# Kernel tuning notes

Measured on AMD Instinct MI355X. Metric: run time of the kernel, lower is better.

## Reference

```python
import jax, jax.numpy as jnp
import numpy as np

B, L, E = 4, 1024, 1024
H, TOPK = 16, 32
DH = E // H


def setup_inputs() -> dict:
    key = jax.random.key(0)
    ks = jax.random.split(key, 11)
    s = 1.0 / np.sqrt(E)
    return {
        "Q": jax.random.normal(ks[0], (B, L, E), jnp.float32),
        "K": jax.random.normal(ks[1], (B, L, E), jnp.float32),
        "V": jax.random.normal(ks[2], (B, L, E), jnp.float32),
        "Wq": jax.random.normal(ks[3], (E, E), jnp.float32) * s,
        "bq": jnp.zeros((E,), jnp.float32),
        "Wk": jax.random.normal(ks[4], (E, E), jnp.float32) * s,
        "bk": jnp.zeros((E,), jnp.float32),
        "Wv": jax.random.normal(ks[5], (E, E), jnp.float32) * s,
        "bv": jnp.zeros((E,), jnp.float32),
        "Wo": jax.random.normal(ks[6], (E, E), jnp.float32) * s,
        "bo": jnp.zeros((E,), jnp.float32),
    }


def reference(Q, K, V, Wq, bq, Wk, bk, Wv, bv, Wo, bo):
    # Linear projections (torch Linear: x @ W.T + b), split heads -> [B,H,L,Dh]
    q = (Q @ Wq.T + bq).reshape(B, L, H, DH).transpose(0, 2, 1, 3)
    k = (K @ Wk.T + bk).reshape(B, L, H, DH).transpose(0, 2, 1, 3)
    v = (V @ Wv.T + bv).reshape(B, L, H, DH).transpose(0, 2, 1, 3)

    # Full attention logits [B,H,L,L]
    logits = jnp.einsum("bhld,bhmd->bhlm", q, k) / np.sqrt(DH)

    # Keep only top-k per query row; rest -> -inf (as in torch scatter_)
    top_vals, top_idx = jax.lax.top_k(logits, TOPK)  # [B,H,L,TOPK]
    bi = jnp.arange(B)[:, None, None, None]
    hi = jnp.arange(H)[None, :, None, None]
    li = jnp.arange(L)[None, None, :, None]
    masked = jnp.full_like(logits, -jnp.inf).at[bi, hi, li, top_idx].set(top_vals)

    attn = jax.nn.softmax(masked, axis=-1)
    out = jnp.einsum("bhlm,bhmd->bhld", attn, v)
    out = out.transpose(0, 2, 1, 3).reshape(B, L, E)
    return out @ Wo.T + bo
```

## Files before the change

kernel.cpp:

```cpp
#include <hip/hip_runtime.h>


typedef short v8s __attribute__((ext_vector_type(8)));
typedef _Float16 v8h __attribute__((ext_vector_type(8)));
typedef float v4f __attribute__((ext_vector_type(4)));

#define B_ 4
#define L_ 1024
#define E_ 1024
#define H_ 16
#define DH_ 64
#define M_ 4096

__device__ __forceinline__ unsigned short f2bf_u(float f) {
    unsigned u = __float_as_uint(f);
    unsigned r = u + 0x7FFFu + ((u >> 16) & 1u);
    return (unsigned short)(r >> 16);
}
__device__ __forceinline__ unsigned short f2h_u(float f) {
    _Float16 h = (_Float16)f;
    union { _Float16 h; unsigned short u; } c; c.h = h; return c.u;
}
__device__ __forceinline__ float h2f_u(unsigned short u) {
    union { _Float16 h; unsigned short u; } c; c.u = u; return (float)c.h;
}
__device__ __forceinline__ unsigned f2key(float f) {
    unsigned u = __float_as_uint(f);
    u = ((int)u < 0) ? ~u : (u | 0x80000000u);
    return u & 0xFFFFFFF0u;
}
__device__ __forceinline__ unsigned f2keyfull(float f) {
    unsigned u = __float_as_uint(f);
    return ((int)u < 0) ? ~u : (u | 0x80000000u);
}
__device__ __forceinline__ float key2f(unsigned k) {
    unsigned u = (k & 0x80000000u) ? (k & 0x7FFFFFFFu) : ~k;
    return __uint_as_float(u);
}
__device__ __forceinline__ float rl_f(float v, int l) {
    return __uint_as_float((unsigned)__builtin_amdgcn_readlane(__float_as_int(v), l));
}
__device__ __forceinline__ int rl_i(int v, int l) {
    return __builtin_amdgcn_readlane(v, l);
}
__device__ __forceinline__ void gload_lds16(const unsigned short* g, unsigned short* l) {
    __builtin_amdgcn_global_load_lds(
        (const __attribute__((address_space(1))) void*)g,
        (__attribute__((address_space(3))) void*)l, 16, 0, 0);
}

__global__ __launch_bounds__(256) void splitH_kernel(
    const float* __restrict__ x, unsigned short* __restrict__ y,
    int n8, int isB, float prescale)
{
    int i = blockIdx.x * 256 + threadIdx.x;
    if (i >= n8) return;
    float4 v0 = *(const float4*)(x + 8*(size_t)i);
    float4 v1 = *(const float4*)(x + 8*(size_t)i + 4);
    float f[8] = {v0.x, v0.y, v0.z, v0.w, v1.x, v1.y, v1.z, v1.w};
    unsigned short o[24];
#pragma unroll
    for (int c = 0; c < 8; ++c) {
        float fv = f[c] * prescale;
        unsigned short h = f2h_u(fv);
        float r = fv - h2f_u(h);
        unsigned short l = f2h_u(r);
        int b = 3*c;
        if (!isB) { o[b] = h; o[b+1] = l; o[b+2] = h; }
        else      { o[b] = h; o[b+1] = h; o[b+2] = l; }
    }
    uint4* dst = (uint4*)(y + 24*(size_t)i);
    const unsigned* ou = (const unsigned*)o;
    dst[0] = make_uint4(ou[0], ou[1], ou[2], ou[3]);
    dst[1] = make_uint4(ou[4], ou[5], ou[6], ou[7]);
    dst[2] = make_uint4(ou[8], ou[9], ou[10], ou[11]);
}

#define STAGE_TILE_GEN(Ap_, Bp_, Abuf_, Bbuf_, kt_)                       \
  {                                                                       \
    const int k0_ = (kt_) << 6;                                           \
    _Pragma("unroll")                                                     \
    for (int c_ = 0; c_ < 2; ++c_) {                                      \
      int lin_ = c_*512 + t;                                              \
      int r_ = lin_ >> 3, s_ = lin_ & 7;                                  \
      gload_lds16(Ap_ + (size_t)(m0 + r_)*K2 + k0_ + ((s_ ^ (r_&7))*8),   \
                  &Abuf_[lin_*8]);                                        \
    }                                                                     \
    _Pragma("unroll")                                                     \
    for (int c_ = 0; c_ < 2; ++c_) {                                      \
      int lin_ = c_*512 + t;                                              \
      int r_ = lin_ >> 3, s_ = lin_ & 7;                                  \
      gload_lds16(Bp_ + (size_t)(n0 + r_)*K2 + k0_ + ((s_ ^ (r_&7))*8),   \
                  &Bbuf_[lin_*8]);                                        \
    }                                                                     \
  }

#define GEMM_COMPUTE(Abuf_, Bbuf_)                                        \
  {                                                                       \
    _Pragma("unroll")                                                     \
    for (int ks = 0; ks < 2; ++ks) {                                      \
        v8h af[2], bf[4];                                                 \
        _Pragma("unroll")                                                 \
        for (int mt = 0; mt < 2; ++mt) {                                  \
            int ra = wrow + mt*16 + l16;                                  \
            int sl = (ks*4 + quad) ^ (ra & 7);                            \
            af[mt] = *(const v8h*)&Abuf_[ra*64 + sl*8];                   \
        }                                                                 \
        _Pragma("unroll")                                                 \
        for (int nt = 0; nt < 4; ++nt) {                                  \
            int rb = wcol + nt*16 + l16;                                  \
            int sl = (ks*4 + quad) ^ (rb & 7);                            \
            bf[nt] = *(const v8h*)&Bbuf_[rb*64 + sl*8];                   \
        }                                                                 \
        _Pragma("unroll")                                                 \
        for (int mt = 0; mt < 2; ++mt)                                    \
            _Pragma("unroll")                                             \
            for (int nt = 0; nt < 4; ++nt)                                \
                acc[mt][nt] = __builtin_amdgcn_mfma_f32_16x16x32_f16(     \
                    af[mt], bf[nt], acc[mt][nt], 0, 0, 0);                \
    }                                                                     \
  }

__global__ __launch_bounds__(512) void gemm_f16(
    const unsigned short* __restrict__ A,
    const unsigned short* __restrict__ Bw,
    const float* __restrict__ bias,
    int K2, int mode, float scale,
    float* __restrict__ outF,
    unsigned short* __restrict__ outB)
{
    __shared__ __align__(16) unsigned short As[3][128*64];
    __shared__ __align__(16) unsigned short Bs[3][128*64];
    const int t    = threadIdx.x;
    const int lane = t & 63;
    const int w    = t >> 6;
    const int quad = lane >> 4;
    const int l16  = lane & 15;
    const int bid  = blockIdx.x;
    const int xcd  = bid & 7;
    const int loc  = bid >> 3;
    const int m0   = (xcd * 4 + (loc & 3)) * 128;
    const int n0   = (loc >> 2) * 128;
    const int wrow = (w >> 1) * 32;
    const int wcol = (w & 1) * 64;

    v4f acc[2][4];
#pragma unroll
    for (int i = 0; i < 2; ++i)
#pragma unroll
        for (int j = 0; j < 4; ++j) acc[i][j] = (v4f){0.f,0.f,0.f,0.f};

    STAGE_TILE_GEN(A, Bw, As[0], Bs[0], 0)
    STAGE_TILE_GEN(A, Bw, As[1], Bs[1], 1)

    const int nk = K2 >> 6;
    for (int ki = 0; ki < nk; ++ki) {
        const int cur = ki % 3;
        asm volatile("s_waitcnt lgkmcnt(0)" ::: "memory");
        __builtin_amdgcn_s_barrier();
        if (ki + 2 < nk) {
            const int nb = (ki + 2) % 3;
            STAGE_TILE_GEN(A, Bw, As[nb], Bs[nb], ki + 2)
        }
        if (ki + 2 < nk)       asm volatile("s_waitcnt vmcnt(8)" ::: "memory");
        else if (ki + 1 < nk)  asm volatile("s_waitcnt vmcnt(4)" ::: "memory");
        else                   asm volatile("s_waitcnt vmcnt(0)" ::: "memory");
        __builtin_amdgcn_s_barrier();
        GEMM_COMPUTE(As[cur], Bs[cur])
    }

#pragma unroll
    for (int nt = 0; nt < 4; ++nt) {
        int n = n0 + wcol + nt*16 + l16;
        float bb = bias[n];
#pragma unroll
        for (int mt = 0; mt < 2; ++mt) {
#pragma unroll
            for (int r = 0; r < 4; ++r) {
                int m = m0 + wrow + mt*16 + quad*4 + r;
                float val = (acc[mt][nt][r] * 0.03125f + bb) * scale;
                if (mode == 0) {
                    outF[(size_t)m * 1024 + n] = val;
                } else {
                    int b = m >> 10, l = m & 1023;
                    int h = n >> 6,  d = n & 63;
                    size_t oidx = (((size_t)(b*16 + h)) * 1024 + l) * 64 + d;
                    outF[oidx] = val;
                    if (mode == 2) outB[oidx] = f2bf_u(val);
                }
            }
        }
    }
}

__global__ __launch_bounds__(512, 4) void gemm_f16_qk(
    const unsigned short* __restrict__ A0,
    const unsigned short* __restrict__ A1,
    const unsigned short* __restrict__ B0,
    const unsigned short* __restrict__ B1,
    const float* __restrict__ bias0,
    const float* __restrict__ bias1,
    float scale0, float scale1,
    float* __restrict__ outF0,
    float* __restrict__ outF1,
    unsigned short* __restrict__ outB0,
    unsigned short* __restrict__ outB1)
{
    __shared__ __align__(16) unsigned short As[2][128*64];
    __shared__ __align__(16) unsigned short Bs[2][128*64];
    const int K2   = 3072;
    const int t    = threadIdx.x;
    const int lane = t & 63;
    const int w    = t >> 6;
    const int quad = lane >> 4;
    const int l16  = lane & 15;
    const int z    = blockIdx.y;
    const unsigned short* A  = z ? A1 : A0;
    const unsigned short* Bw = z ? B1 : B0;
    const float* bias        = z ? bias1 : bias0;
    const float scale        = z ? scale1 : scale0;
    float* outF              = z ? outF1 : outF0;
    unsigned short* outB     = z ? outB1 : outB0;

    const int bid  = blockIdx.x;
    const int xcd  = bid & 7;
    const int loc  = bid >> 3;
    const int m0   = (xcd * 4 + (loc & 3)) * 128;
    const int n0   = (loc >> 2) * 128;
    const int wrow = (w >> 1) * 32;
    const int wcol = (w & 1) * 64;

    v4f acc[2][4];
#pragma unroll
    for (int i = 0; i < 2; ++i)
#pragma unroll
        for (int j = 0; j < 4; ++j) acc[i][j] = (v4f){0.f,0.f,0.f,0.f};

    STAGE_TILE_GEN(A, Bw, As[0], Bs[0], 0)

    const int nk = K2 >> 6;
    for (int ki = 0; ki < nk; ++ki) {
        const int cur = ki & 1;
        __syncthreads();
        if (ki + 1 < nk) {
            STAGE_TILE_GEN(A, Bw, As[cur ^ 1], Bs[cur ^ 1], ki + 1)
        }
        GEMM_COMPUTE(As[cur], Bs[cur])
    }

#pragma unroll
    for (int nt = 0; nt < 4; ++nt) {
        int n = n0 + wcol + nt*16 + l16;
        float bb = bias[n];
#pragma unroll
        for (int mt = 0; mt < 2; ++mt) {
#pragma unroll
            for (int r = 0; r < 4; ++r) {
                int m = m0 + wrow + mt*16 + quad*4 + r;
                float val = (acc[mt][nt][r] * 0.03125f + bb) * scale;
                int b = m >> 10, l = m & 1023;
                int h = n >> 6,  d = n & 63;
                size_t oidx = (((size_t)(b*16 + h)) * 1024 + l) * 64 + d;
                outF[oidx] = val;
                outB[oidx] = f2bf_u(val);
            }
        }
    }
}


#define SEL_STEP(s_, BUF)                                              \
  {                                                                    \
    v8s b0_ = BUF[0], b1_ = BUF[1];                                    \
    if ((s_) + 2 < 4) {                                                \
      BUF[0] = *(const v8s*)(kbase + ((s_)+2)*16384);                  \
      BUF[1] = *(const v8s*)(kbase + ((s_)+2)*16384 + 32);             \
    }                                                                  \
    v4f a0_ = (v4f){0.f,0.f,0.f,0.f};                                  \
    v4f a1_ = (v4f){0.f,0.f,0.f,0.f};                                  \
    a0_ = __builtin_amdgcn_mfma_f32_16x16x32_bf16(afrA[0], b0_, a0_, 0,0,0); \
    a0_ = __builtin_amdgcn_mfma_f32_16x16x32_bf16(afrA[1], b1_, a0_, 0,0,0); \
    a1_ = __builtin_amdgcn_mfma_f32_16x16x32_bf16(afrB[0], b0_, a1_, 0,0,0); \
    a1_ = __builtin_amdgcn_mfma_f32_16x16x32_bf16(afrB[1], b1_, a1_, 0,0,0); \
    if (quad < 2) {                                                    \
      _Pragma("unroll")                                                \
      for (int r_ = 0; r_ < 4; ++r_)                                   \
        sbig[(quad*4 + r_)*1044 + (s_)*256 + w*16 + l16] = a0_[r_];    \
      _Pragma("unroll")                                                \
      for (int r_ = 0; r_ < 4; ++r_)                                   \
        sbig[(8 + quad*4 + r_)*1044 + (s_)*256 + w*16 + l16] = a1_[r_];\
    }                                                                  \
  }

__global__ __launch_bounds__(1024, 4) void attn_sel(
    const unsigned short* __restrict__ qb,
    const unsigned short* __restrict__ kb,
    unsigned short* __restrict__ candB,
    unsigned* __restrict__ cntB)
{
    __shared__ __align__(16) unsigned short qbs[16*72];
    __shared__ __align__(16) float sbig[16*1044];

    const int t    = threadIdx.x;
    const int lane = t & 63;
    const int w    = t >> 6;
    const int quad = lane >> 4;
    const int l16  = lane & 15;

    const int blk = blockIdx.x;
    const int jj  = blk >> 3;
    const int bh  = (blk & 7) * 8 + (jj >> 6);
    const int qt  = jj & 63;
    const int l0  = qt * 16;
    const size_t kvB = (size_t)bh * 1024;

    if (t < 128) {
        int r2 = t >> 3, cc2 = t & 7;
        *(uint4*)&qbs[r2*72 + cc2*8] = *(const uint4*)&qb[(kvB + l0 + r2)*64 + cc2*8];
    }
    __syncthreads();
    v8s afrA[2], afrB[2];
#pragma unroll
    for (int ks = 0; ks < 2; ++ks) {
        afrA[ks] = *(const v8s*)&qbs[(l16 & 7)*72 + ks*32 + quad*8];
        afrB[ks] = *(const v8s*)&qbs[(8 + (l16 & 7))*72 + ks*32 + quad*8];
    }

    const unsigned short* kbase = kb + (kvB + w*16 + l16) * 64 + quad*8;
    v8s buf0[2], buf1[2];
    buf0[0] = *(const v8s*)(kbase);         buf0[1] = *(const v8s*)(kbase + 32);
    buf1[0] = *(const v8s*)(kbase + 16384); buf1[1] = *(const v8s*)(kbase + 16384 + 32);
    SEL_STEP(0, buf0) SEL_STEP(1, buf1)
    SEL_STEP(2, buf0) SEL_STEP(3, buf1)
    __syncthreads();

    unsigned skey[16];
#pragma unroll
    for (int kt = 0; kt < 16; ++kt) {
        float sv = sbig[w*1044 + kt*64 + lane];
        unsigned u = __float_as_uint(sv);
        u = ((int)u < 0) ? ~u : (u | 0x80000000u);
        skey[kt] = (u & 0xFFFFFFF0u) | (unsigned)kt;
    }

    unsigned kmax = 0;
#pragma unroll
    for (int kt = 0; kt < 16; ++kt) kmax = max(kmax, skey[kt]);
#pragma unroll
    for (int off = 32; off; off >>= 1)
        kmax = max(kmax, (unsigned)__shfl_xor((int)kmax, off));
    float fm = key2f(kmax);

    unsigned tau = 0; bool ok = false;
    if (fm > 0.f) {
        float lof = 0.28f * fm, hif = 0.88f * fm;
        for (int it = 0; it < 12; ++it) {
            float midf = 0.5f * (lof + hif);
            unsigned tk = f2key(midf);
            int c = 0;
#pragma unroll
            for (int kt = 0; kt < 16; ++kt)
                c += (int)__popcll(__ballot(skey[kt] >= tk));
            tau = tk;
            if (c <= 64 && c >= 36) { ok = true; break; }
            if (c > 64) lof = midf; else hif = midf;
        }
    }
    if (!ok) {
        unsigned lo = 0u, hi = 0xFFFFFFFFu;
        for (int it = 0; ; ++it) {
            unsigned mid = lo + ((hi - lo) >> 1);
            int c = 0;
#pragma unroll
            for (int kt = 0; kt < 16; ++kt)
                c += (int)__popcll(__ballot(skey[kt] >= mid));
            tau = mid;
            if (it >= 33 || (c <= 64 && c >= 36)) break;
            if (c > 64) lo = mid + 1; else hi = mid - 1;
        }
    }

    const size_t row = kvB + l0 + w;
    int base = 0;
#pragma unroll
    for (int kt = 0; kt < 16; ++kt) {
        bool f = skey[kt] >= tau;
        unsigned long long mk = __ballot(f);
        if (f) {
            int pos = base + (int)__popcll(mk & ((1ull << lane) - 1ull));
            if (pos < 64) candB[row*64 + pos] = (unsigned short)(kt*64 + lane);
        }
        base += (int)__popcll(mk);
    }
    if (lane == 0) cntB[row] = (unsigned)(base > 64 ? 64 : base);
}


#define LDGRP(base_, PV, LV)                                          \
  {                                                                   \
    _Pragma("unroll")                                                 \
    for (int u = 0; u < 8; ++u) {                                     \
      int idx_ = (base_) + u;                                         \
      float pt_ = rl_f(pc, idx_);                                     \
      int   ci_ = rl_i(cc, idx_);                                     \
      bool  vv_ = idx_ < nnz;                                         \
      PV[u] = vv_ ? pt_ : 0.f;                                        \
      LV[u] = vbase[(size_t)(vv_ ? ci_ : 0) * 64];                    \
    }                                                                 \
  }

__global__ __launch_bounds__(1024, 4) void attn_out(
    const float* __restrict__ qf,
    const float* __restrict__ kf,
    const float* __restrict__ vf,
    const unsigned short* __restrict__ candB,
    const unsigned* __restrict__ cntB,
    unsigned short* __restrict__ outX3)
{
    __shared__ __align__(16) float qfs[16*68];

    const int t    = threadIdx.x;
    const int lane = t & 63;
    const int w    = t >> 6;

    const int blk = blockIdx.x;
    const int jj  = blk >> 3;
    const int bh  = (blk & 7) * 8 + (jj >> 6);
    const int qt  = jj & 63;
    const int l0  = qt * 16;
    const size_t kvB = (size_t)bh * 1024;

    const int qrow = w;
    const size_t row = kvB + l0 + w;

    const int cnum = (int)cntB[row];
    const int cj_raw = (int)candB[row*64 + lane];

    if (t < 256) {
        int r2 = t >> 4, c4 = (t & 15) * 4;
        *(float4*)&qfs[r2*68 + c4] = *(const float4*)&qf[(kvB + l0 + r2)*64 + c4];
    }
    __syncthreads();

    int cj = 0x3FFFFFFF;
    float ef = -INFINITY;
    {
        const int cjs = (lane < cnum) ? cj_raw : 0;
        const float* kr = kf + (kvB + cjs) * 64;
        double s0 = 0.0, s1 = 0.0;
#pragma unroll
        for (int d4 = 0; d4 < 16; d4 += 2) {
            float4 qa = *(const float4*)&qfs[qrow*68 + d4*4];
            float4 ka = *(const float4*)&kr[d4*4];
            float4 qb2 = *(const float4*)&qfs[qrow*68 + d4*4 + 4];
            float4 kb2 = *(const float4*)&kr[d4*4 + 4];
            s0 += (double)qa.x * ka.x; s0 += (double)qa.y * ka.y;
            s0 += (double)qa.z * ka.z; s0 += (double)qa.w * ka.w;
            s1 += (double)qb2.x * kb2.x; s1 += (double)qb2.y * kb2.y;
            s1 += (double)qb2.z * kb2.z; s1 += (double)qb2.w * kb2.w;
        }
        if (lane < cnum) { cj = cj_raw; ef = (float)(s0 + s1); }
    }

    const unsigned uf = f2keyfull(ef);
    unsigned T = 0u;
#pragma unroll
    for (int b = 31; b >= 0; --b) {
        unsigned cndt = T | (1u << b);
        int c = (int)__popcll(__ballot(uf >= cndt));
        if (c >= 32) T = cndt;
    }
    float e31 = key2f(T);
    int c_ge = (int)__popcll(__ballot(uf >= T));

    float mx = ef;
    float tm = (uf < T) ? ef : -INFINITY;
#pragma unroll
    for (int off = 32; off; off >>= 1) {
        mx = fmaxf(mx, __shfl_xor(mx, off));
        tm = fmaxf(tm, __shfl_xor(tm, off));
    }
    float e32v = (c_ge >= 33) ? e31 : tm;

    float cmid = 0.5f * (e31 + e32v);
    const float btau = 1.5e-5f;
    bool certain = (ef > cmid + btau);
    bool band    = (fabsf(ef - cmid) <= btau);
    int A = (int)__popcll(__ballot(certain));
    int m = (int)__popcll(__ballot(band));
    float wgt = band ? ((float)(32 - A) / (float)m) : (certain ? 1.f : 0.f);

    float p = wgt * __expf(ef - mx);
    float Z = p;
#pragma unroll
    for (int off = 32; off; off >>= 1) Z += __shfl_xor(Z, off);

    bool sel = (wgt > 0.f);
    unsigned long long mk = __ballot(sel);
    int nnz = (int)__popcll(mk);
    unsigned long long lt = (1ull << lane) - 1ull;
    int pos = sel ? (int)__popcll(mk & lt)
                  : nnz + (int)__popcll(~mk & lt);
    float pc = __uint_as_float((unsigned)__builtin_amdgcn_ds_permute(
                   pos << 2, __float_as_int(p)));
    int   cc = __builtin_amdgcn_ds_permute(pos << 2, cj);

    const float* vbase = vf + kvB * 64 + lane;
    int ng = (nnz + 7) >> 3;
    float pA[8], lA[8], pB[8], lB[8];
    float oa = 0.f, ob = 0.f, oc = 0.f, od = 0.f;
    LDGRP(0, pA, lA)
    int g = 0;
    for (;;) {
        if (g + 1 < ng) LDGRP((g+1)*8, pB, lB)
        oa += pA[0]*lA[0]; ob += pA[1]*lA[1]; oc += pA[2]*lA[2]; od += pA[3]*lA[3];
        oa += pA[4]*lA[4]; ob += pA[5]*lA[5]; oc += pA[6]*lA[6]; od += pA[7]*lA[7];
        ++g; if (g >= ng) break;
        if (g + 1 < ng) LDGRP((g+1)*8, pA, lA)
        oa += pB[0]*lB[0]; ob += pB[1]*lB[1]; oc += pB[2]*lB[2]; od += pB[3]*lB[3];
        oa += pB[4]*lB[4]; ob += pB[5]*lB[5]; oc += pB[6]*lB[6]; od += pB[7]*lB[7];
        ++g; if (g >= ng) break;
    }
    float o = (oa + ob) + (oc + od);
    float oval = o / Z;

    unsigned short hh = f2h_u(oval);
    float rres = oval - h2f_u(hh);
    unsigned short ll = f2h_u(rres);
    int lq = l0 + qrow;
    size_t e = ((size_t)(bh >> 4) * 1024 + lq) * 1024 + (bh & 15) * 64 + lane;
    outX3[3*e]     = hh;
    outX3[3*e + 1] = ll;
    outX3[3*e + 2] = hh;
}

extern "C" void kernel_launch(void* const* d_in, const int* in_sizes, int n_in,
                              void* d_out, int out_size, void* d_ws, size_t ws_size,
                              hipStream_t stream)
{
    const float* Q  = (const float*)d_in[0];
    const float* K  = (const float*)d_in[1];
    const float* V  = (const float*)d_in[2];
    const float* Wq = (const float*)d_in[3];
    const float* bq = (const float*)d_in[4];
    const float* Wk = (const float*)d_in[5];
    const float* bk = (const float*)d_in[6];
    const float* Wv = (const float*)d_in[7];
    const float* bv = (const float*)d_in[8];
    const float* Wo = (const float*)d_in[9];
    const float* bo = (const float*)d_in[10];
    float* out = (float*)d_out;

    if (ws_size < 115343360) return;

    char* ws = (char*)d_ws;
    unsigned short* X3a = (unsigned short*)(ws + 0);
    unsigned short* X3b = (unsigned short*)(ws + 25165824);
    float* vf = (float*)(ws + 25165824);
    unsigned short* candB = (unsigned short*)(ws + 41943040);
    unsigned* cntB = (unsigned*)(ws + 50331648);
    unsigned short* W3a = (unsigned short*)(ws + 50331648);
    unsigned short* W3b = (unsigned short*)(ws + 56623104);
    float* qf = (float*)(ws + 62914560);
    float* kf = (float*)(ws + 79691776);
    unsigned short* qb = (unsigned short*)(ws + 96468992);
    unsigned short* kb = (unsigned short*)(ws + 104857600);

    const int nX8 = M_ * E_ / 8;
    const int nW8 = E_ * E_ / 8;
    dim3 blk(256);
    dim3 blkG(512);
    dim3 gG(256);
    dim3 gQK(256, 2);
    dim3 gX(nX8 / 256), gW(nW8 / 256);

    splitH_kernel<<<gX, blk, 0, stream>>>(Q, X3a, nX8, 0, 1.0f);
    splitH_kernel<<<gX, blk, 0, stream>>>(K, X3b, nX8, 0, 1.0f);
    splitH_kernel<<<gW, blk, 0, stream>>>(Wq, W3a, nW8, 1, 32.0f);
    splitH_kernel<<<gW, blk, 0, stream>>>(Wk, W3b, nW8, 1, 32.0f);
    gemm_f16_qk<<<gQK, blkG, 0, stream>>>(X3a, X3b, W3a, W3b, bq, bk,
                                          0.125f, 1.0f, qf, kf, qb, kb);
    splitH_kernel<<<gX, blk, 0, stream>>>(V, X3a, nX8, 0, 1.0f);
    splitH_kernel<<<gW, blk, 0, stream>>>(Wv, W3b, nW8, 1, 32.0f);
    gemm_f16<<<gG, blkG, 0, stream>>>(X3a, W3b, bv, 3072, 1, 1.0f, vf, nullptr);
    attn_sel<<<dim3(4096), dim3(1024), 0, stream>>>(qb, kb, candB, cntB);
    attn_out<<<dim3(4096), dim3(1024), 0, stream>>>(qf, kf, vf, candB, cntB, X3a);
    splitH_kernel<<<gW, blk, 0, stream>>>(Wo, W3b, nW8, 1, 32.0f);
    gemm_f16<<<gG, blkG, 0, stream>>>(X3a, W3b, bo, 3072, 0, 1.0f, out, nullptr);
}
```

Baseline: 513.4 us.

## Merge V projection GEMM and attention selection into one heterogeneous launch

```diff
diff --git a/kernel.cpp b/kernel.cpp
--- a/kernel.cpp
+++ b/kernel.cpp
@@ -292,22 +292,107 @@
     }                                                                  \
   }
 
-__global__ __launch_bounds__(1024, 4) void attn_sel(
+__global__ __launch_bounds__(1024, 8) void vsel_kernel(
+    const unsigned short* __restrict__ A,
+    const unsigned short* __restrict__ Bw,
+    const float* __restrict__ bias,
+    float* __restrict__ outF,
     const unsigned short* __restrict__ qb,
     const unsigned short* __restrict__ kb,
     unsigned short* __restrict__ candB,
     unsigned* __restrict__ cntB)
 {
-    __shared__ __align__(16) unsigned short qbs[16*72];
-    __shared__ __align__(16) float sbig[16*1044];
-
+    __shared__ __align__(16) char smem[69120];
     const int t    = threadIdx.x;
     const int lane = t & 63;
     const int w    = t >> 6;
     const int quad = lane >> 4;
     const int l16  = lane & 15;
 
-    const int blk = blockIdx.x;
+    if (blockIdx.x < 256) {
+        unsigned short* As0 = (unsigned short*)smem;
+        unsigned short* As1 = (unsigned short*)(smem + 16384);
+        unsigned short* Bs0 = (unsigned short*)(smem + 32768);
+        unsigned short* Bs1 = (unsigned short*)(smem + 49152);
+        const int bid  = blockIdx.x;
+        const int xcd  = bid & 7;
+        const int loc  = bid >> 3;
+        const int m0   = (xcd * 4 + (loc & 3)) * 128;
+        const int n0   = (loc >> 2) * 128;
+        const int wrow = (w >> 2) * 32;
+        const int wcol = (w & 3) * 32;
+
+        v4f acc[2][2];
+#pragma unroll
+        for (int i = 0; i < 2; ++i)
+#pragma unroll
+            for (int j = 0; j < 2; ++j) acc[i][j] = (v4f){0.f,0.f,0.f,0.f};
+
+        const int r_ = t >> 3, s_ = t & 7;
+        const unsigned short* Arow = A  + (size_t)(m0 + r_) * 3072 + (s_ ^ (r_ & 7)) * 8;
+        const unsigned short* Brow = Bw + (size_t)(n0 + r_) * 3072 + (s_ ^ (r_ & 7)) * 8;
+
+        gload_lds16(Arow, &As0[t*8]);
+        gload_lds16(Brow, &Bs0[t*8]);
+
+        for (int ki = 0; ki < 48; ++ki) {
+            const int cur = ki & 1;
+            __syncthreads();
+            if (ki + 1 < 48) {
+                const int k0 = (ki + 1) << 6;
+                gload_lds16(Arow + k0, cur ? &As0[t*8] : &As1[t*8]);
+                gload_lds16(Brow + k0, cur ? &Bs0[t*8] : &Bs1[t*8]);
+            }
+            const unsigned short* Ab = cur ? As1 : As0;
+            const unsigned short* Bb = cur ? Bs1 : Bs0;
+#pragma unroll
+            for (int ks = 0; ks < 2; ++ks) {
+                v8h af[2], bf[2];
+#pragma unroll
+                for (int mt = 0; mt < 2; ++mt) {
+                    int ra = wrow + mt*16 + l16;
+                    int sl = (ks*4 + quad) ^ (ra & 7);
+                    af[mt] = *(const v8h*)&Ab[ra*64 + sl*8];
+                }
+#pragma unroll
+                for (int nt = 0; nt < 2; ++nt) {
+                    int rb = wcol + nt*16 + l16;
+                    int sl = (ks*4 + quad) ^ (rb & 7);
+                    bf[nt] = *(const v8h*)&Bb[rb*64 + sl*8];
+                }
+#pragma unroll
+                for (int mt = 0; mt < 2; ++mt)
+#pragma unroll
+                    for (int nt = 0; nt < 2; ++nt)
+                        acc[mt][nt] = __builtin_amdgcn_mfma_f32_16x16x32_f16(
+                            af[mt], bf[nt], acc[mt][nt], 0, 0, 0);
+            }
+        }
+
+#pragma unroll
+        for (int nt = 0; nt < 2; ++nt) {
+            int n = n0 + wcol + nt*16 + l16;
+            float bb = bias[n];
+#pragma unroll
+            for (int mt = 0; mt < 2; ++mt) {
+#pragma unroll
+                for (int r = 0; r < 4; ++r) {
+                    int m = m0 + wrow + mt*16 + quad*4 + r;
+                    float val = acc[mt][nt][r] * 0.03125f + bb;
+                    int b = m >> 10, l = m & 1023;
+                    int h = n >> 6,  d = n & 63;
+                    size_t oidx = (((size_t)(b*16 + h)) * 1024 + l) * 64 + d;
+                    outF[oidx] = val;
+                }
+            }
+        }
+        return;
+    }
+
+    unsigned short* qbs = (unsigned short*)smem;
+    float* sbig = (float*)(smem + 2304);
+
+    const int blk = blockIdx.x - 256;
     const int jj  = blk >> 3;
     const int bh  = (blk & 7) * 8 + (jj >> 6);
     const int qt  = jj & 63;
@@ -582,8 +667,8 @@
                                           0.125f, 1.0f, qf, kf, qb, kb);
     splitH_kernel<<<gX, blk, 0, stream>>>(V, X3a, nX8, 0, 1.0f);
     splitH_kernel<<<gW, blk, 0, stream>>>(Wv, W3b, nW8, 1, 32.0f);
-    gemm_f16<<<gG, blkG, 0, stream>>>(X3a, W3b, bv, 3072, 1, 1.0f, vf, nullptr);
-    attn_sel<<<dim3(4096), dim3(1024), 0, stream>>>(qb, kb, candB, cntB);
+    vsel_kernel<<<dim3(4352), dim3(1024), 0, stream>>>(
+        X3a, W3b, bv, vf, qb, kb, candB, cntB);
     attn_out<<<dim3(4096), dim3(1024), 0, stream>>>(qf, kf, vf, candB, cntB, X3a);
     splitH_kernel<<<gW, blk, 0, stream>>>(Wo, W3b, nW8, 1, 32.0f);
     gemm_f16<<<gG, blkG, 0, stream>>>(X3a, W3b, bo, 3072, 0, 1.0f, out, nullptr);
```

Measured after the change: 505.0 us. No clear change (-1.6%).
